# Optimization experiments

Hardware: AMD Instinct MI355X
Metric: run time of the kernel (lower is better)

## Reference

```python
import jax, jax.numpy as jnp
import numpy as np
from jax import lax

# ---- config (mirrors cfg) ----
NUM_LEVELS = 4
DS = 2            # DS_FACTOR
T = 16            # TILE_SIZE
SR = 4            # SEARCH_RADIUS
PADD = 1
SW = 0.1          # SPATIAL_WEIGHT
GR = 2            # GAUSS_RADIUS
SIGMA = 1.0
SS = 2 * (SR + PADD) + 1      # 11: padded search grid
SSC = 2 * SR + 1              # 9: cropped search grid
WIN = T + 2 * (SR + PADD)     # 26: gathered window per tile

# ---- subpixel-refinement quadratic-fit filters (from __init__) ----
F_A11 = jnp.asarray(np.array([[1,-2,1],[2,-4,2],[1,-2,1]], np.float32) / 4.0)
F_A22 = jnp.asarray(np.array([[1,2,1],[-2,-4,-2],[1,2,1]], np.float32) / 4.0)
F_A12 = jnp.asarray(np.array([[1,0,-1],[0,0,0],[-1,0,1]], np.float32) / 4.0)
F_B1  = jnp.asarray(np.array([[-1,0,1],[-2,0,2],[-1,0,1]], np.float32) / 8.0)
F_B2  = jnp.asarray(np.array([[-1,-2,-1],[0,0,0],[1,2,1]], np.float32) / 8.0)
F_C   = jnp.asarray(np.array([[-1,2,-1],[2,12,2],[-1,2,-1]], np.float32) / 16.0)


def _gauss_kernel():
    ws = 2 * GR + 1
    ax = np.arange(ws, dtype=np.float32) - GR
    g = np.exp(-(ax ** 2) / (2.0 * SIGMA ** 2))
    k = np.outer(g, g)
    k = k / k.sum()
    return jnp.asarray(k, jnp.float32)


def _pyramid(x):
    """Gaussian pyramid: depthwise gaussian blur + avg-pool(ds) per level."""
    k = _gauss_kernel()[None, None]  # OIHW, C=1
    pad = (2 * GR + 1 - 1) // 2
    pyr = [x]
    for _ in range(NUM_LEVELS - 1):
        y = lax.conv_general_dilated(x, k, (1, 1), [(pad, pad), (pad, pad)],
                                     dimension_numbers=('NCHW', 'OIHW', 'NCHW'))
        n, c, h, w = y.shape
        x = y.reshape(n, c, h // DS, DS, w // DS, DS).mean(axis=(3, 5))
        pyr.append(x)
    return pyr


def _sdist_map():
    ax = (np.arange(SS, dtype=np.float32) - (SR + PADD)) / float(SS)
    return jnp.asarray(ax[:, None] ** 2 + ax[None, :] ** 2, jnp.float32)


def _step(init_offset, src, dst):
    """One pyramid-level block-matching step + subpixel refine."""
    n, nth, ntw, _ = init_offset.shape
    H, W = src.shape[2], src.shape[3]
    oy = jnp.round(init_offset[..., 0]).astype(jnp.int32)
    ox = jnp.round(init_offset[..., 1]).astype(jnp.int32)
    base_y = (jnp.arange(nth, dtype=jnp.int32) * T)[None, :, None]
    base_x = (jnp.arange(ntw, dtype=jnp.int32) * T)[None, None, :]
    y0 = base_y + oy - (SR + PADD)
    x0 = base_x + ox - (SR + PADD)
    Y = jnp.clip(y0[..., None] + jnp.arange(WIN), 0, H - 1)
    X = jnp.clip(x0[..., None] + jnp.arange(WIN), 0, W - 1)
    nidx = jnp.arange(n)[:, None, None, None, None]
    window = dst[:, 0][nidx, Y[..., :, None], X[..., None, :]]
    # source tiles [n,nth,ntw,T,T]
    src_t = src[:, 0].reshape(n, nth, T, ntw, T).transpose(0, 1, 3, 2, 4)
    # all SSxSS candidate tiles from the window (static slide indices)
    sl = jnp.arange(SS)[:, None] + jnp.arange(T)[None, :]  # [SS,T]
    cand = window[:, :, :, sl[:, None, :, None], sl[None, :, None, :]]  # [n,nth,ntw,SS,SS,T,T]
    adist = jnp.mean((cand - src_t[:, :, :, None, None]) ** 2, axis=(-2, -1))
    dist_full = adist + SW * _sdist_map()  # [n,nth,ntw,SS,SS]
    dist = dist_full[:, :, :, PADD:-PADD, PADD:-PADD].reshape(n, nth, ntw, SSC * SSC)
    min_dist = jnp.min(dist, axis=3)
    pk = jnp.argmin(dist, axis=3)
    py = pk // SSC
    px = pk % SSC
    offset = init_offset + jnp.stack([(py - SR).astype(jnp.float32),
                                      (px - SR).astype(jnp.float32)], axis=3)
    # RegionSelection: 3x3 neighborhood of dist_full around (py+PADD, px+PADD)
    ry = (py + PADD)[..., None] + jnp.arange(-1, 2)
    rx = (px + PADD)[..., None] + jnp.arange(-1, 2)
    tyi = jnp.arange(nth)[None, :, None, None, None]
    txi = jnp.arange(ntw)[None, None, :, None, None]
    yreg = dist_full[nidx, tyi, txi, ry[..., :, None], rx[..., None, :]]  # [n,nth,ntw,3,3]
    s = lambda f: jnp.sum(f * yreg, axis=(-2, -1))
    a11 = jax.nn.relu(s(F_A11))
    a22 = jax.nn.relu(s(F_A22))
    a12 = s(F_A12)
    b1 = s(F_B1)
    b2 = s(F_B2)
    det = a11 * a22 - a12 ** 2
    a12z = jnp.where(det < 0, jnp.zeros_like(a12), a12)
    mu_x = -(a22 * b1 - a12z * b2) / det
    mu_y = -(a11 * b2 - a12z * b1) / det
    mu_len = jnp.sqrt(mu_y ** 2 + mu_x ** 2)
    dx = jnp.where(mu_len < 1.0, mu_x, jnp.zeros_like(mu_x))
    dy = jnp.where(mu_len < 1.0, mu_y, jnp.zeros_like(mu_y))
    offset = offset.at[..., 0].add(dy).at[..., 1].add(dx)
    return offset, min_dist


def _inherit(prev_offset, nth, ntw, H, W):
    typ = jnp.arange(nth) // DS
    txp = jnp.arange(ntw) // DS
    off = DS * prev_offset[:, typ[:, None], txp[None, :], :]
    iy = (jnp.arange(nth, dtype=jnp.float32) * T)[None, :, None]
    ix = (jnp.arange(ntw, dtype=jnp.float32) * T)[None, None, :]
    dy = jnp.clip(off[..., 0] + iy, 0.0, float(H - T)) - iy
    dx = jnp.clip(off[..., 1] + ix, 0.0, float(W - T)) - ix
    return jnp.round(jnp.stack([dy, dx], axis=3))


def _align(src, dst):
    ps = _pyramid(src)
    pd = _pyramid(dst)
    offset = None
    min_dist = None
    for level in range(NUM_LEVELS - 1, -1, -1):
        s, d = ps[level], pd[level]
        n, _, h, w = s.shape
        nth = int(np.ceil(h / T))
        ntw = int(np.ceil(w / T))
        if level == NUM_LEVELS - 1:
            init = jnp.zeros((n, nth, ntw, 2), jnp.float32)
        else:
            init = _inherit(offset, nth, ntw, h, w)
        offset, min_dist = _step(init, s, d)
    # nearest-neighbor upsample by TILE_SIZE to per-pixel maps
    pixel_off = jnp.repeat(jnp.repeat(offset, T, axis=1), T, axis=2)   # [n,H,W,2]
    pixel_dist = jnp.repeat(jnp.repeat(min_dist, T, axis=1), T, axis=2)  # [n,H,W]
    return pixel_off, pixel_dist


def setup_inputs() -> dict:
    key = jax.random.key(0)
    k1, k2 = jax.random.split(key)
    src = jax.random.uniform(k1, (4, 1, 512, 512), jnp.float32)
    dst = jax.random.uniform(k2, (4, 1, 512, 512), jnp.float32)
    return {"src": src, "dst": dst}


def reference(src, dst):
    return _align(src, dst)
```

## Files before the change

### kernel.cpp

```cpp
#include <hip/hip_runtime.h>


#define NB 4
#define NPIX (NB * 512 * 512)

constexpr float H6[6] = {
    0.027244342f, 0.149345013f, 0.323410645f,
    0.323410645f, 0.149345013f, 0.027244342f
};

__global__ void __launch_bounds__(256, 4)
pyramid_kernel(const float* __restrict__ src, const float* __restrict__ dst,
               float* __restrict__ ws) {
    __shared__ float smem[5520];
    float* patch = smem;
    float* tmpH1 = smem + 3840;
    float* l1    = smem;
    float* tmpH2 = smem + 784;
    float* l2    = smem + 1120;
    float* tmpH3 = smem + 1264;

    float* sL1 = ws;
    float* dL1 = sL1 + 4 * 65536;
    float* sL2 = dL1 + 4 * 65536;
    float* dL2 = sL2 + 4 * 16384;
    float* sL3 = dL2 + 4 * 16384;
    float* dL3 = sL3 + 4 * 4096;

    const int bx = blockIdx.x, by = blockIdx.y, z = blockIdx.z;
    const int t = threadIdx.x;
    const float* in = (z < 4) ? (src + (size_t)z * 262144) : (dst + (size_t)(z - 4) * 262144);
    float* oL1 = ((z < 4) ? sL1 : dL1) + (size_t)(z & 3) * 65536;
    float* oL2 = ((z < 4) ? sL2 : dL2) + (size_t)(z & 3) * 16384;
    float* oL3 = ((z < 4) ? sL3 : dL3) + (size_t)(z & 3) * 4096;

    {
        const int oy = by * 32 - 14, ox = bx * 32 - 14;
        for (int idx = t; idx < 3600; idx += 256) {
            int r = idx / 60, c = idx - r * 60;
            int gy = oy + r, gx = ox + c;
            float v = 0.f;
            if ((unsigned)gy < 512u && (unsigned)gx < 512u) v = in[gy * 512 + gx];
            patch[r * 64 + c] = v;
        }
    }
    __syncthreads();
    for (int idx = t; idx < 1680; idx += 256) {
        int r = idx / 28, v = idx - r * 28;
        const float* p = &patch[r * 64 + 2 * v];
        float a = 0.f;
        #pragma unroll
        for (int bq = 0; bq < 6; ++bq) a = fmaf(H6[bq], p[bq], a);
        tmpH1[r * 28 + v] = a;
    }
    __syncthreads();
    {
        const int oy = by * 16 - 6, ox = bx * 16 - 6;
        for (int idx = t; idx < 784; idx += 256) {
            int u = idx / 28, v = idx - u * 28;
            float a = 0.f;
            int y1 = oy + u, x1 = ox + v;
            if ((unsigned)y1 < 256u && (unsigned)x1 < 256u) {
                #pragma unroll
                for (int bq = 0; bq < 6; ++bq) a = fmaf(H6[bq], tmpH1[(2 * u + bq) * 28 + v], a);
            }
            l1[u * 28 + v] = a;
        }
    }
    __syncthreads();
    {
        int u = t >> 4, v = t & 15;
        oL1[(by * 16 + u) * 256 + bx * 16 + v] = l1[(6 + u) * 28 + 6 + v];
    }
    for (int idx = t; idx < 336; idx += 256) {
        int r = idx / 12, v = idx - r * 12;
        const float* p = &l1[r * 28 + 2 * v];
        float a = 0.f;
        #pragma unroll
        for (int bq = 0; bq < 6; ++bq) a = fmaf(H6[bq], p[bq], a);
        tmpH2[r * 12 + v] = a;
    }
    __syncthreads();
    {
        const int oy = by * 8 - 2, ox = bx * 8 - 2;
        if (t < 144) {
            int u = t / 12, v = t - u * 12;
            float a = 0.f;
            int y2 = oy + u, x2 = ox + v;
            if ((unsigned)y2 < 128u && (unsigned)x2 < 128u) {
                #pragma unroll
                for (int bq = 0; bq < 6; ++bq) a = fmaf(H6[bq], tmpH2[(2 * u + bq) * 12 + v], a);
            }
            l2[u * 12 + v] = a;
        }
    }
    __syncthreads();
    if (t < 64) {
        int u = t >> 3, v = t & 7;
        oL2[(by * 8 + u) * 128 + bx * 8 + v] = l2[(2 + u) * 12 + 2 + v];
    } else if (t < 112) {
        int idx = t - 64;
        int r = idx >> 2, v = idx & 3;
        const float* p = &l2[r * 12 + 2 * v];
        float a = 0.f;
        #pragma unroll
        for (int bq = 0; bq < 6; ++bq) a = fmaf(H6[bq], p[bq], a);
        tmpH3[r * 4 + v] = a;
    }
    __syncthreads();
    if (t < 16) {
        int u = t >> 2, v = t & 3;
        float a = 0.f;
        #pragma unroll
        for (int bq = 0; bq < 6; ++bq) a = fmaf(H6[bq], tmpH3[(2 * u + bq) * 4 + v], a);
        oL3[(by * 4 + u) * 64 + bx * 4 + v] = a;
    }
}

__device__ __forceinline__ void inherit_off(int ty, int tx, int H,
                                            float pary, float parx,
                                            float& dyf, float& dxf) {
    float iy = (float)(ty * 16), ix = (float)(tx * 16);
    dyf = rintf(fminf(fmaxf(2.f * pary + iy, 0.f), (float)(H - 16)) - iy);
    dxf = rintf(fminf(fmaxf(2.f * parx + ix, 0.f), (float)(H - 16)) - ix);
}

template<int NL>
__device__ __forceinline__ void load_win(const float* __restrict__ dimg, int H,
                                         int y0, int x0, float* win, int lt) {
    for (int idx = lt; idx < 676; idx += NL) {
        int r = idx / 26, c = idx - r * 26;
        int gy = min(max(y0 + r, 0), H - 1);
        int gx = min(max(x0 + c, 0), H - 1);
        win[r * 28 + c] = dimg[gy * H + gx];
    }
}

template<bool FULL>
__device__ __forceinline__ void ssd_dist(const float* win, const float* st,
                                         float* dist, int lt) {
    const int dy = FULL ? (lt >> 4) : (lt >> 3);
    if (dy < 11) {
        float acc[11];
        #pragma unroll
        for (int q = 0; q < 11; ++q) acc[q] = 0.f;
        constexpr int ROWS = FULL ? 1 : 2;
        #pragma unroll
        for (int rr = 0; rr < ROWS; ++rr) {
            const int i = FULL ? (lt & 15) : ((lt & 7) * 2 + rr);
            float w[28], s[16];
            const float4* wp = (const float4*)&win[(dy + i) * 28];
            #pragma unroll
            for (int q = 0; q < 7; ++q) ((float4*)w)[q] = wp[q];
            const float4* sp = (const float4*)&st[i * 16];
            #pragma unroll
            for (int q = 0; q < 4; ++q) ((float4*)s)[q] = sp[q];
            #pragma unroll
            for (int dx = 0; dx < 11; ++dx) {
                #pragma unroll
                for (int j = 0; j < 16; ++j) {
                    float d = w[dx + j] - s[j];
                    acc[dx] = fmaf(d, d, acc[dx]);
                }
            }
        }
        constexpr int MMAX = FULL ? 8 : 4;
        #pragma unroll
        for (int m = 1; m <= MMAX; m <<= 1) {
            #pragma unroll
            for (int dx = 0; dx < 11; ++dx) acc[dx] += __shfl_xor(acc[dx], m);
        }
        const bool leader = FULL ? ((lt & 15) == 0) : ((lt & 7) == 0);
        if (leader) {
            float ay = (float)(dy - 5) * (1.f / 11.f);
            #pragma unroll
            for (int dx = 0; dx < 11; ++dx) {
                float ax = (float)(dx - 5) * (1.f / 11.f);
                dist[dy * 11 + dx] = acc[dx] * (1.f / 256.f) + 0.1f * (ay * ay + ax * ax);
            }
        }
    }
}

__device__ __forceinline__ void argmin_refine(const float* dist, int lt,
                                              float dyf, float dxf,
                                              float& roy, float& rox, float& rod) {
    const int l = lt & 63;
    float bv; int bk;
    {
        int k = l;
        int py = k / 9, px = k - (k / 9) * 9;
        bv = dist[(py + 1) * 11 + (px + 1)]; bk = k;
        k = l + 64;
        if (k < 81) {
            py = k / 9; px = k - (k / 9) * 9;
            float d = dist[(py + 1) * 11 + (px + 1)];
            if (d < bv) { bv = d; bk = k; }
        }
    }
    #pragma unroll
    for (int m = 1; m <= 32; m <<= 1) {
        float ov = __shfl_xor(bv, m);
        int   ok = __shfl_xor(bk, m);
        if (ov < bv || (ov == bv && ok < bk)) { bv = ov; bk = ok; }
    }
    {
        int py = bk / 9, px = bk - (bk / 9) * 9;
        float y00 = dist[(py + 0) * 11 + (px + 0)], y01 = dist[(py + 0) * 11 + (px + 1)], y02 = dist[(py + 0) * 11 + (px + 2)];
        float y10 = dist[(py + 1) * 11 + (px + 0)], y11 = dist[(py + 1) * 11 + (px + 1)], y12 = dist[(py + 1) * 11 + (px + 2)];
        float y20 = dist[(py + 2) * 11 + (px + 0)], y21 = dist[(py + 2) * 11 + (px + 1)], y22 = dist[(py + 2) * 11 + (px + 2)];

        float a11 = (y00 - 2.f * y01 + y02 + 2.f * y10 - 4.f * y11 + 2.f * y12 + y20 - 2.f * y21 + y22) * 0.25f;
        a11 = fmaxf(a11, 0.f);
        float a22 = (y00 + 2.f * y01 + y02 - 2.f * y10 - 4.f * y11 - 2.f * y12 + y20 + 2.f * y21 + y22) * 0.25f;
        a22 = fmaxf(a22, 0.f);
        float a12 = (y00 - y02 - y20 + y22) * 0.25f;
        float b1  = (-y00 + y02 - 2.f * y10 + 2.f * y12 - y20 + y22) * 0.125f;
        float b2  = (-y00 - 2.f * y01 - y02 + y20 + 2.f * y21 + y22) * 0.125f;

        float det  = a11 * a22 - a12 * a12;
        float a12z = (det < 0.f) ? 0.f : a12;
        float mu_x = -(a22 * b1 - a12z * b2) / det;
        float mu_y = -(a11 * b2 - a12z * b1) / det;
        float mu_len = sqrtf(mu_x * mu_x + mu_y * mu_y);
        float addx = (mu_len < 1.f) ? mu_x : 0.f;
        float addy = (mu_len < 1.f) ? mu_y : 0.f;

        roy = dyf + (float)(py - 4) + addy;
        rox = dxf + (float)(px - 4) + addx;
        rod = bv;
    }
}

__global__ void __launch_bounds__(256, 4)
step_chain_kernel(const float* __restrict__ src, const float* __restrict__ dst,
                  const float* __restrict__ ws, float* __restrict__ out) {
    __shared__ float smem[6072];

    const float* sL1 = ws;
    const float* dL1 = sL1 + 4 * 65536;
    const float* sL2 = dL1 + 4 * 65536;
    const float* dL2 = sL2 + 4 * 16384;
    const float* sL3 = dL2 + 4 * 16384;
    const float* dL3 = sL3 + 4 * 4096;

    const int gid = blockIdx.x;
    const int b   = gid >> 8;
    const int ty1 = (gid >> 4) & 15;
    const int tx1 = gid & 15;
    const int t    = threadIdx.x;
    const int slot = t >> 7;
    const int s_t  = t & 127;

    float* win_c = smem;
    float* dist_c = smem + 3640;
    float* winA  = smem + 728 + (2 * slot + 0) * 728;
    float* winB  = smem + 728 + (2 * slot + 1) * 728;
    float* distA = smem + 3768 + (2 * slot + 0) * 128;
    float* distB = smem + 3768 + (2 * slot + 1) * 128;
    float* stL3 = smem + 4280;
    float* stL2 = smem + 4536;
    float* stL1 = smem + 4792;
    float* st0  = smem + 5048;

    const float* s0 = src + (size_t)b * 262144; const float* d0 = dst + (size_t)b * 262144;
    const float* s1 = sL1 + (size_t)b * 65536;  const float* d1 = dL1 + (size_t)b * 65536;
    const float* s2 = sL2 + (size_t)b * 16384;  const float* d2 = dL2 + (size_t)b * 16384;
    const float* s3 = sL3 + (size_t)b * 4096;   const float* d3 = dL3 + (size_t)b * 4096;

    {
        const int it = t & 63, r = it >> 2, q = t & 3;
        const int c = t >> 6;
        const int ty0 = 2 * ty1 + (c >> 1), tx0 = 2 * tx1 + (c & 1);
        const float4* p0 = (const float4*)(s0 + (size_t)(ty0 * 16 + r) * 512 + tx0 * 16);
        ((float4*)&st0[c * 256 + r * 16])[q] = p0[q];
        if (t < 64) {
            const float4* p = (const float4*)(s3 + (size_t)((ty1 >> 2) * 16 + r) * 64 + (tx1 >> 2) * 16);
            ((float4*)&stL3[r * 16])[q] = p[q];
        } else if (t < 128) {
            const float4* p = (const float4*)(s2 + (size_t)((ty1 >> 1) * 16 + r) * 128 + (tx1 >> 1) * 16);
            ((float4*)&stL2[r * 16])[q] = p[q];
        } else if (t < 192) {
            const float4* p = (const float4*)(s1 + (size_t)(ty1 * 16 + r) * 256 + tx1 * 16);
            ((float4*)&stL1[r * 16])[q] = p[q];
        }
    }

    float oy, ox, od;
    {
        load_win<256>(d3, 64, (ty1 >> 2) * 16 - 5, (tx1 >> 2) * 16 - 5, win_c, t);
        __syncthreads();
        ssd_dist<true>(win_c, stL3, dist_c, t);
        __syncthreads();
        argmin_refine(dist_c, t, 0.f, 0.f, oy, ox, od);
    }
    {
        float dyf, dxf; inherit_off(ty1 >> 1, tx1 >> 1, 128, oy, ox, dyf, dxf);
        load_win<256>(d2, 128, (ty1 >> 1) * 16 + (int)dyf - 5, (tx1 >> 1) * 16 + (int)dxf - 5, win_c, t);
        __syncthreads();
        ssd_dist<true>(win_c, stL2, dist_c, t);
        __syncthreads();
        argmin_refine(dist_c, t, dyf, dxf, oy, ox, od);
    }
    {
        float dyf, dxf; inherit_off(ty1, tx1, 256, oy, ox, dyf, dxf);
        load_win<256>(d1, 256, ty1 * 16 + (int)dyf - 5, tx1 * 16 + (int)dxf - 5, win_c, t);
        __syncthreads();
        ssd_dist<true>(win_c, stL1, dist_c, t);
        __syncthreads();
        argmin_refine(dist_c, t, dyf, dxf, oy, ox, od);
    }

    const int tyA = 2 * ty1,     txA = 2 * tx1 + slot;
    const int tyB = 2 * ty1 + 1, txB = 2 * tx1 + slot;
    float dyfA, dxfA, dyfB, dxfB;
    inherit_off(tyA, txA, 512, oy, ox, dyfA, dxfA);
    inherit_off(tyB, txB, 512, oy, ox, dyfB, dxfB);
    load_win<128>(d0, 512, tyA * 16 + (int)dyfA - 5, txA * 16 + (int)dxfA - 5, winA, s_t);
    load_win<128>(d0, 512, tyB * 16 + (int)dyfB - 5, txB * 16 + (int)dxfB - 5, winB, s_t);
    __syncthreads();
    ssd_dist<false>(winA, st0 + (0 * 2 + slot) * 256, distA, s_t);
    __syncthreads();
    ssd_dist<false>(winB, st0 + (1 * 2 + slot) * 256, distB, s_t);
    __syncthreads();

    const int r = s_t >> 3, c2 = (s_t & 7) * 2;
    {
        float oyA, oxA, odA;
        argmin_refine(distA, s_t, dyfA, dxfA, oyA, oxA, odA);
        int pyy = tyA * 16 + r, pxx = txA * 16 + c2;
        size_t pi = ((size_t)(b * 512 + pyy)) * 512 + pxx;
        float2 o; o.x = oyA; o.y = oxA;
        ((float2*)out)[pi]     = o;
        ((float2*)out)[pi + 1] = o;
        float2 dd; dd.x = odA; dd.y = odA;
        *(float2*)(out + (size_t)NPIX * 2 + pi) = dd;
    }
    {
        float oyB, oxB, odB;
        argmin_refine(distB, s_t, dyfB, dxfB, oyB, oxB, odB);
        int pyy = tyB * 16 + r, pxx = txB * 16 + c2;
        size_t pi = ((size_t)(b * 512 + pyy)) * 512 + pxx;
        float2 o; o.x = oyB; o.y = oxB;
        ((float2*)out)[pi]     = o;
        ((float2*)out)[pi + 1] = o;
        float2 dd; dd.x = odB; dd.y = odB;
        *(float2*)(out + (size_t)NPIX * 2 + pi) = dd;
    }
}

extern "C" void kernel_launch(void* const* d_in, const int* in_sizes, int n_in,
                              void* d_out, int out_size, void* d_ws, size_t ws_size,
                              hipStream_t stream) {
    const float* src = (const float*)d_in[0];
    const float* dst = (const float*)d_in[1];
    float* out = (float*)d_out;
    float* ws  = (float*)d_ws;

    hipLaunchKernelGGL(pyramid_kernel, dim3(16, 16, 8), dim3(256), 0, stream, src, dst, ws);
    hipLaunchKernelGGL(step_chain_kernel, dim3(1024), dim3(256), 0, stream, src, dst, ws, out);
}
```

Before: 111.1 us.

## Prefetch next pyramid level's search superset into LDS during current SSD

Each level of the coarse-to-fine chain now issues the global load for a clamped superset region of the next level's destination image into shared memory before running the current level's SSD, so global latency overlaps with compute. Per-level windows are then copied from this LDS superset at offsets derived from the inherited displacement. The full-resolution level loads one 62x62 superset that serves all four subtiles instead of four separate gathers. This depends on the inherited offsets staying inside the superset bounds, and it raises shared memory use to about 40 KB per block, which may limit occupancy.

```diff
diff --git a/kernel.cpp b/kernel.cpp
--- a/kernel.cpp
+++ b/kernel.cpp
@@ -125,14 +125,23 @@
     dxf = rintf(fminf(fmaxf(2.f * parx + ix, 0.f), (float)(H - 16)) - ix);
 }
 
+template<int NL, int SPAN>
+__device__ __forceinline__ void load_super(const float* __restrict__ dimg, int H,
+                                           int By, int Bx, float* sup, int lt) {
+    for (int idx = lt; idx < SPAN * SPAN; idx += NL) {
+        int r = idx / SPAN, c = idx - r * SPAN;
+        int gy = min(max(By + r, 0), H - 1);
+        int gx = min(max(Bx + c, 0), H - 1);
+        sup[r * 62 + c] = dimg[gy * H + gx];
+    }
+}
+
 template<int NL>
-__device__ __forceinline__ void load_win(const float* __restrict__ dimg, int H,
-                                         int y0, int x0, float* win, int lt) {
+__device__ __forceinline__ void copy_win(const float* sup, int offr, int offc,
+                                         float* win, int lt) {
     for (int idx = lt; idx < 676; idx += NL) {
         int r = idx / 26, c = idx - r * 26;
-        int gy = min(max(y0 + r, 0), H - 1);
-        int gx = min(max(x0 + c, 0), H - 1);
-        win[r * 28 + c] = dimg[gy * H + gx];
+        win[r * 28 + c] = sup[(offr + r) * 62 + offc + c];
     }
 }
 
@@ -235,7 +244,7 @@
 __global__ void __launch_bounds__(256, 4)
 step_chain_kernel(const float* __restrict__ src, const float* __restrict__ dst,
                   const float* __restrict__ ws, float* __restrict__ out) {
-    __shared__ float smem[6072];
+    __shared__ float smem[9920];
 
     const float* sL1 = ws;
     const float* dL1 = sL1 + 4 * 65536;
@@ -252,16 +261,17 @@
     const int slot = t >> 7;
     const int s_t  = t & 127;
 
-    float* win_c = smem;
+    float* win_c  = smem;
+    float* winA   = smem + 728 + (2 * slot + 0) * 728;
+    float* winB   = smem + 728 + (2 * slot + 1) * 728;
     float* dist_c = smem + 3640;
-    float* winA  = smem + 728 + (2 * slot + 0) * 728;
-    float* winB  = smem + 728 + (2 * slot + 1) * 728;
-    float* distA = smem + 3768 + (2 * slot + 0) * 128;
-    float* distB = smem + 3768 + (2 * slot + 1) * 128;
+    float* distA  = smem + 3768 + (2 * slot + 0) * 128;
+    float* distB  = smem + 3768 + (2 * slot + 1) * 128;
     float* stL3 = smem + 4280;
     float* stL2 = smem + 4536;
     float* stL1 = smem + 4792;
     float* st0  = smem + 5048;
+    float* sup  = smem + 6072;
 
     const float* s0 = src + (size_t)b * 262144; const float* d0 = dst + (size_t)b * 262144;
     const float* s1 = sL1 + (size_t)b * 65536;  const float* d1 = dL1 + (size_t)b * 65536;
@@ -285,39 +295,54 @@
             ((float4*)&stL1[r * 16])[q] = p[q];
         }
     }
+    {
+        const int y0 = (ty1 >> 2) * 16 - 5, x0 = (tx1 >> 2) * 16 - 5;
+        for (int idx = t; idx < 676; idx += 256) {
+            int r = idx / 26, c = idx - r * 26;
+            int gy = min(max(y0 + r, 0), 63);
+            int gx = min(max(x0 + c, 0), 63);
+            win_c[r * 28 + c] = d3[gy * 64 + gx];
+        }
+    }
+    load_super<256, 46>(d2, 128, (ty1 >> 1) * 16 - 15, (tx1 >> 1) * 16 - 15, sup, t);
+    __syncthreads();
 
     float oy, ox, od;
-    {
-        load_win<256>(d3, 64, (ty1 >> 2) * 16 - 5, (tx1 >> 2) * 16 - 5, win_c, t);
-        __syncthreads();
-        ssd_dist<true>(win_c, stL3, dist_c, t);
-        __syncthreads();
-        argmin_refine(dist_c, t, 0.f, 0.f, oy, ox, od);
-    }
-    {
-        float dyf, dxf; inherit_off(ty1 >> 1, tx1 >> 1, 128, oy, ox, dyf, dxf);
-        load_win<256>(d2, 128, (ty1 >> 1) * 16 + (int)dyf - 5, (tx1 >> 1) * 16 + (int)dxf - 5, win_c, t);
-        __syncthreads();
-        ssd_dist<true>(win_c, stL2, dist_c, t);
-        __syncthreads();
-        argmin_refine(dist_c, t, dyf, dxf, oy, ox, od);
-    }
-    {
-        float dyf, dxf; inherit_off(ty1, tx1, 256, oy, ox, dyf, dxf);
-        load_win<256>(d1, 256, ty1 * 16 + (int)dyf - 5, tx1 * 16 + (int)dxf - 5, win_c, t);
-        __syncthreads();
-        ssd_dist<true>(win_c, stL1, dist_c, t);
-        __syncthreads();
-        argmin_refine(dist_c, t, dyf, dxf, oy, ox, od);
-    }
+    ssd_dist<true>(win_c, stL3, dist_c, t);
+    __syncthreads();
+    argmin_refine(dist_c, t, 0.f, 0.f, oy, ox, od);
+
+    float dyf2, dxf2;
+    inherit_off(ty1 >> 1, tx1 >> 1, 128, oy, ox, dyf2, dxf2);
+    copy_win<256>(sup, (int)dyf2 + 10, (int)dxf2 + 10, win_c, t);
+    __syncthreads();
+    load_super<256, 46>(d1, 256, ty1 * 16 + 2 * (int)dyf2 - 15,
+                        tx1 * 16 + 2 * (int)dxf2 - 15, sup, t);
+    ssd_dist<true>(win_c, stL2, dist_c, t);
+    __syncthreads();
+    argmin_refine(dist_c, t, dyf2, dxf2, oy, ox, od);
+
+    float dyf1, dxf1;
+    inherit_off(ty1, tx1, 256, oy, ox, dyf1, dxf1);
+    copy_win<256>(sup, (int)dyf1 - 2 * (int)dyf2 + 10,
+                  (int)dxf1 - 2 * (int)dxf2 + 10, win_c, t);
+    __syncthreads();
+    const int Brow0 = 32 * ty1 + 2 * (int)dyf1 - 15;
+    const int Bcol0 = 32 * tx1 + 2 * (int)dxf1 - 15;
+    load_super<256, 62>(d0, 512, Brow0, Bcol0, sup, t);
+    ssd_dist<true>(win_c, stL1, dist_c, t);
+    __syncthreads();
+    argmin_refine(dist_c, t, dyf1, dxf1, oy, ox, od);
 
     const int tyA = 2 * ty1,     txA = 2 * tx1 + slot;
     const int tyB = 2 * ty1 + 1, txB = 2 * tx1 + slot;
     float dyfA, dxfA, dyfB, dxfB;
     inherit_off(tyA, txA, 512, oy, ox, dyfA, dxfA);
     inherit_off(tyB, txB, 512, oy, ox, dyfB, dxfB);
-    load_win<128>(d0, 512, tyA * 16 + (int)dyfA - 5, txA * 16 + (int)dxfA - 5, winA, s_t);
-    load_win<128>(d0, 512, tyB * 16 + (int)dyfB - 5, txB * 16 + (int)dxfB - 5, winB, s_t);
+    copy_win<128>(sup, (tyA * 16 + (int)dyfA - 5) - Brow0,
+                  (txA * 16 + (int)dxfA - 5) - Bcol0, winA, s_t);
+    copy_win<128>(sup, (tyB * 16 + (int)dyfB - 5) - Brow0,
+                  (txB * 16 + (int)dxfB - 5) - Bcol0, winB, s_t);
     __syncthreads();
     ssd_dist<false>(winA, st0 + (0 * 2 + slot) * 256, distA, s_t);
     __syncthreads();
```

New measurement: 114.5 us. 1.03x slower.

## Split step-chain blocks into 128-thread halves, recomputing coarse levels per half

Applied to the files above, without the earlier changes.

Each block of the step-chain kernel is split into two 128-thread blocks, giving twice as many blocks. Each block handles one column of level-0 tiles and recomputes the coarse levels 3..1 chain on its own. The aim is more, smaller blocks with lower shared memory so more can be resident, and fewer threads per __syncthreads barrier. In exchange the coarse-level search work and window loads are duplicated across the two halves. Each coarse SSD also uses the 2-rows-per-thread path with 128 threads instead of 1 row with 256.

```diff
diff --git a/kernel.cpp b/kernel.cpp
--- a/kernel.cpp
+++ b/kernel.cpp
@@ -125,10 +125,9 @@
     dxf = rintf(fminf(fmaxf(2.f * parx + ix, 0.f), (float)(H - 16)) - ix);
 }
 
-template<int NL>
-__device__ __forceinline__ void load_win(const float* __restrict__ dimg, int H,
-                                         int y0, int x0, float* win, int lt) {
-    for (int idx = lt; idx < 676; idx += NL) {
+__device__ __forceinline__ void load_win128(const float* __restrict__ dimg, int H,
+                                            int y0, int x0, float* win, int lt) {
+    for (int idx = lt; idx < 676; idx += 128) {
         int r = idx / 26, c = idx - r * 26;
         int gy = min(max(y0 + r, 0), H - 1);
         int gx = min(max(x0 + c, 0), H - 1);
@@ -136,18 +135,16 @@
     }
 }
 
-template<bool FULL>
-__device__ __forceinline__ void ssd_dist(const float* win, const float* st,
-                                         float* dist, int lt) {
-    const int dy = FULL ? (lt >> 4) : (lt >> 3);
+__device__ __forceinline__ void ssd_dist128(const float* win, const float* st,
+                                            float* dist, int lt) {
+    const int dy = lt >> 3;
     if (dy < 11) {
         float acc[11];
         #pragma unroll
         for (int q = 0; q < 11; ++q) acc[q] = 0.f;
-        constexpr int ROWS = FULL ? 1 : 2;
-        #pragma unroll
-        for (int rr = 0; rr < ROWS; ++rr) {
-            const int i = FULL ? (lt & 15) : ((lt & 7) * 2 + rr);
+        #pragma unroll
+        for (int rr = 0; rr < 2; ++rr) {
+            const int i = (lt & 7) * 2 + rr;
             float w[28], s[16];
             const float4* wp = (const float4*)&win[(dy + i) * 28];
             #pragma unroll
@@ -164,14 +161,12 @@
                 }
             }
         }
-        constexpr int MMAX = FULL ? 8 : 4;
-        #pragma unroll
-        for (int m = 1; m <= MMAX; m <<= 1) {
+        #pragma unroll
+        for (int m = 1; m <= 4; m <<= 1) {
             #pragma unroll
             for (int dx = 0; dx < 11; ++dx) acc[dx] += __shfl_xor(acc[dx], m);
         }
-        const bool leader = FULL ? ((lt & 15) == 0) : ((lt & 7) == 0);
-        if (leader) {
+        if ((lt & 7) == 0) {
             float ay = (float)(dy - 5) * (1.f / 11.f);
             #pragma unroll
             for (int dx = 0; dx < 11; ++dx) {
@@ -232,10 +227,10 @@
     }
 }
 
-__global__ void __launch_bounds__(256, 4)
+__global__ void __launch_bounds__(128, 4)
 step_chain_kernel(const float* __restrict__ src, const float* __restrict__ dst,
                   const float* __restrict__ ws, float* __restrict__ out) {
-    __shared__ float smem[6072];
+    __shared__ float smem[3848];
 
     const float* sL1 = ws;
     const float* dL1 = sL1 + 4 * 65536;
@@ -245,89 +240,89 @@
     const float* dL3 = sL3 + 4 * 4096;
 
     const int gid = blockIdx.x;
-    const int b   = gid >> 8;
-    const int ty1 = (gid >> 4) & 15;
-    const int tx1 = gid & 15;
-    const int t    = threadIdx.x;
-    const int slot = t >> 7;
-    const int s_t  = t & 127;
-
-    float* win_c = smem;
-    float* dist_c = smem + 3640;
-    float* winA  = smem + 728 + (2 * slot + 0) * 728;
-    float* winB  = smem + 728 + (2 * slot + 1) * 728;
-    float* distA = smem + 3768 + (2 * slot + 0) * 128;
-    float* distB = smem + 3768 + (2 * slot + 1) * 128;
-    float* stL3 = smem + 4280;
-    float* stL2 = smem + 4536;
-    float* stL1 = smem + 4792;
-    float* st0  = smem + 5048;
+    const int b   = gid >> 9;
+    const int ty1 = (gid >> 5) & 15;
+    const int tx1 = (gid >> 1) & 15;
+    const int h   = gid & 1;
+    const int t   = threadIdx.x;
+
+    float* win_c  = smem;
+    float* winA   = smem + 728;
+    float* winB   = smem + 1456;
+    float* dist_c = smem + 2184;
+    float* distA  = smem + 2312;
+    float* distB  = smem + 2440;
+    float* stL3 = smem + 2568;
+    float* stL2 = smem + 2824;
+    float* stL1 = smem + 3080;
+    float* st0A = smem + 3336;
+    float* st0B = smem + 3592;
 
     const float* s0 = src + (size_t)b * 262144; const float* d0 = dst + (size_t)b * 262144;
     const float* s1 = sL1 + (size_t)b * 65536;  const float* d1 = dL1 + (size_t)b * 65536;
     const float* s2 = sL2 + (size_t)b * 16384;  const float* d2 = dL2 + (size_t)b * 16384;
     const float* s3 = sL3 + (size_t)b * 4096;   const float* d3 = dL3 + (size_t)b * 4096;
 
-    {
-        const int it = t & 63, r = it >> 2, q = t & 3;
-        const int c = t >> 6;
-        const int ty0 = 2 * ty1 + (c >> 1), tx0 = 2 * tx1 + (c & 1);
-        const float4* p0 = (const float4*)(s0 + (size_t)(ty0 * 16 + r) * 512 + tx0 * 16);
-        ((float4*)&st0[c * 256 + r * 16])[q] = p0[q];
+    const int tyA = 2 * ty1,     txA = 2 * tx1 + h;
+    const int tyB = 2 * ty1 + 1, txB = 2 * tx1 + h;
+
+    {
+        const int it = t & 63, r = it >> 2, q = it & 3;
         if (t < 64) {
-            const float4* p = (const float4*)(s3 + (size_t)((ty1 >> 2) * 16 + r) * 64 + (tx1 >> 2) * 16);
-            ((float4*)&stL3[r * 16])[q] = p[q];
-        } else if (t < 128) {
-            const float4* p = (const float4*)(s2 + (size_t)((ty1 >> 1) * 16 + r) * 128 + (tx1 >> 1) * 16);
-            ((float4*)&stL2[r * 16])[q] = p[q];
-        } else if (t < 192) {
-            const float4* p = (const float4*)(s1 + (size_t)(ty1 * 16 + r) * 256 + tx1 * 16);
-            ((float4*)&stL1[r * 16])[q] = p[q];
+            const float4* p3 = (const float4*)(s3 + (size_t)((ty1 >> 2) * 16 + r) * 64 + (tx1 >> 2) * 16);
+            ((float4*)&stL3[r * 16])[q] = p3[q];
+            const float4* p1 = (const float4*)(s1 + (size_t)(ty1 * 16 + r) * 256 + tx1 * 16);
+            ((float4*)&stL1[r * 16])[q] = p1[q];
+            const float4* pA = (const float4*)(s0 + (size_t)(tyA * 16 + r) * 512 + txA * 16);
+            ((float4*)&st0A[r * 16])[q] = pA[q];
+        } else {
+            const float4* p2 = (const float4*)(s2 + (size_t)((ty1 >> 1) * 16 + r) * 128 + (tx1 >> 1) * 16);
+            ((float4*)&stL2[r * 16])[q] = p2[q];
+            const float4* pB = (const float4*)(s0 + (size_t)(tyB * 16 + r) * 512 + txB * 16);
+            ((float4*)&st0B[r * 16])[q] = pB[q];
         }
     }
 
     float oy, ox, od;
-    {
-        load_win<256>(d3, 64, (ty1 >> 2) * 16 - 5, (tx1 >> 2) * 16 - 5, win_c, t);
+    load_win128(d3, 64, (ty1 >> 2) * 16 - 5, (tx1 >> 2) * 16 - 5, win_c, t);
+    __syncthreads();
+    ssd_dist128(win_c, stL3, dist_c, t);
+    __syncthreads();
+    argmin_refine(dist_c, t, 0.f, 0.f, oy, ox, od);
+
+    {
+        float dyf, dxf; inherit_off(ty1 >> 1, tx1 >> 1, 128, oy, ox, dyf, dxf);
+        load_win128(d2, 128, (ty1 >> 1) * 16 + (int)dyf - 5, (tx1 >> 1) * 16 + (int)dxf - 5, win_c, t);
         __syncthreads();
-        ssd_dist<true>(win_c, stL3, dist_c, t);
-        __syncthreads();
-        argmin_refine(dist_c, t, 0.f, 0.f, oy, ox, od);
-    }
-    {
-        float dyf, dxf; inherit_off(ty1 >> 1, tx1 >> 1, 128, oy, ox, dyf, dxf);
-        load_win<256>(d2, 128, (ty1 >> 1) * 16 + (int)dyf - 5, (tx1 >> 1) * 16 + (int)dxf - 5, win_c, t);
-        __syncthreads();
-        ssd_dist<true>(win_c, stL2, dist_c, t);
+        ssd_dist128(win_c, stL2, dist_c, t);
         __syncthreads();
         argmin_refine(dist_c, t, dyf, dxf, oy, ox, od);
     }
+
     {
         float dyf, dxf; inherit_off(ty1, tx1, 256, oy, ox, dyf, dxf);
-        load_win<256>(d1, 256, ty1 * 16 + (int)dyf - 5, tx1 * 16 + (int)dxf - 5, win_c, t);
+        load_win128(d1, 256, ty1 * 16 + (int)dyf - 5, tx1 * 16 + (int)dxf - 5, win_c, t);
         __syncthreads();
-        ssd_dist<true>(win_c, stL1, dist_c, t);
+        ssd_dist128(win_c, stL1, dist_c, t);
         __syncthreads();
         argmin_refine(dist_c, t, dyf, dxf, oy, ox, od);
     }
 
-    const int tyA = 2 * ty1,     txA = 2 * tx1 + slot;
-    const int tyB = 2 * ty1 + 1, txB = 2 * tx1 + slot;
     float dyfA, dxfA, dyfB, dxfB;
     inherit_off(tyA, txA, 512, oy, ox, dyfA, dxfA);
     inherit_off(tyB, txB, 512, oy, ox, dyfB, dxfB);
-    load_win<128>(d0, 512, tyA * 16 + (int)dyfA - 5, txA * 16 + (int)dxfA - 5, winA, s_t);
-    load_win<128>(d0, 512, tyB * 16 + (int)dyfB - 5, txB * 16 + (int)dxfB - 5, winB, s_t);
-    __syncthreads();
-    ssd_dist<false>(winA, st0 + (0 * 2 + slot) * 256, distA, s_t);
-    __syncthreads();
-    ssd_dist<false>(winB, st0 + (1 * 2 + slot) * 256, distB, s_t);
-    __syncthreads();
-
-    const int r = s_t >> 3, c2 = (s_t & 7) * 2;
+    load_win128(d0, 512, tyA * 16 + (int)dyfA - 5, txA * 16 + (int)dxfA - 5, winA, t);
+    load_win128(d0, 512, tyB * 16 + (int)dyfB - 5, txB * 16 + (int)dxfB - 5, winB, t);
+    __syncthreads();
+    ssd_dist128(winA, st0A, distA, t);
+    __syncthreads();
+    ssd_dist128(winB, st0B, distB, t);
+    __syncthreads();
+
+    const int r = t >> 3, c2 = (t & 7) * 2;
     {
         float oyA, oxA, odA;
-        argmin_refine(distA, s_t, dyfA, dxfA, oyA, oxA, odA);
+        argmin_refine(distA, t, dyfA, dxfA, oyA, oxA, odA);
         int pyy = tyA * 16 + r, pxx = txA * 16 + c2;
         size_t pi = ((size_t)(b * 512 + pyy)) * 512 + pxx;
         float2 o; o.x = oyA; o.y = oxA;
@@ -338,7 +333,7 @@
     }
     {
         float oyB, oxB, odB;
-        argmin_refine(distB, s_t, dyfB, dxfB, oyB, oxB, odB);
+        argmin_refine(distB, t, dyfB, dxfB, oyB, oxB, odB);
         int pyy = tyB * 16 + r, pxx = txB * 16 + c2;
         size_t pi = ((size_t)(b * 512 + pyy)) * 512 + pxx;
         float2 o; o.x = oyB; o.y = oxB;
@@ -358,5 +353,5 @@
     float* ws  = (float*)d_ws;
 
     hipLaunchKernelGGL(pyramid_kernel, dim3(16, 16, 8), dim3(256), 0, stream, src, dst, ws);
-    hipLaunchKernelGGL(step_chain_kernel, dim3(1024), dim3(256), 0, stream, src, dst, ws, out);
-}
+    hipLaunchKernelGGL(step_chain_kernel, dim3(2048), dim3(128), 0, stream, src, dst, ws, out);
+}
```

New measurement: 120.5 us. +8.4%, slower.
